# Kernel tuning notes

Measured on AMD Instinct MI355X. Metric: run time of the kernel, lower is better.

Reference implementation:

```python
import jax, jax.numpy as jnp
import numpy as np

ALPHA = 0.25
GAMMA = 2.0
DELTA = 0.5
BREAK_W = 1.0
REG_W = 1.0
CLASS_WEIGHT_TABLE = jnp.array([1.0, 4.0, 3.0, 2.0], dtype=jnp.float32)  # classes 0..3
LOG_CLAMP = -100.0  # torch BCELoss clamps log terms at -100

B, T = 2048, 16384


def setup_inputs() -> dict:
    key = jax.random.key(0)
    k1, k2, k3, k4 = jax.random.split(key, 4)
    break_predictions = jax.random.uniform(k1, (B, T), dtype=jnp.float32)
    regression_predictions = jax.random.uniform(k2, (B, T), dtype=jnp.float32) * 3.0
    break_targets = jax.random.uniform(k3, (B, T), dtype=jnp.float32)
    regression_targets = jax.random.uniform(k4, (B, T), dtype=jnp.float32) * 3.0
    return {
        "break_predictions": break_predictions,
        "regression_predictions": regression_predictions,
        "break_targets": break_targets,
        "regression_targets": regression_targets,
    }


def _bce(p, t):
    # torch BCELoss: mean of -(t*log(p) + (1-t)*log(1-p)), logs clamped at -100
    log_p = jnp.maximum(jnp.log(p), LOG_CLAMP)
    log_1p = jnp.maximum(jnp.log1p(-p), LOG_CLAMP)
    return jnp.mean(-(t * log_p + (1.0 - t) * log_1p))


def _duration_aware_focal(y_pred, y_true):
    y_pred = y_pred.reshape(-1)
    y_true = y_true.reshape(-1)
    # class-weight gather: round + clamp to [0,3], index a 4-entry table
    cls_idx = jnp.clip(jnp.round(y_true), 0.0, 3.0).astype(jnp.int32)
    weights = CLASS_WEIGHT_TABLE[cls_idx]
    d = jnp.abs(y_pred - y_true)
    focal = jnp.clip(d / DELTA, 0.0, 1.0) ** GAMMA
    # smooth L1 with beta=DELTA
    base = jnp.where(d < DELTA, 0.5 * d * d / DELTA, d - 0.5 * DELTA)
    return jnp.mean(ALPHA * focal * base * weights)


def reference(break_predictions, regression_predictions, break_targets, regression_targets):
    bt = jnp.clip(break_targets, 0.0, 1.0)
    bp = jnp.clip(break_predictions, 0.0, 1.0)
    break_loss = _bce(bp, bt)
    regression_loss = _duration_aware_focal(regression_predictions, regression_targets)
    total = BREAK_W * break_loss + REG_W * regression_loss
    return (total, break_loss, regression_loss)
```

## Files before the change

kernel.cpp:

```cpp
#include <hip/hip_runtime.h>


constexpr int BLOCK = 256;
constexpr int GRID  = 2048;

__device__ __forceinline__ void accum_elem(float pv, float tv, float qv, float sv,
                                           float& accB, float& accR) {
    constexpr float LN2 = 0.6931471805599453f;
    float pc = fminf(fmaxf(pv, 0.0f), 1.0f);
    float tc = fminf(fmaxf(tv, 0.0f), 1.0f);
    float lp  = fmaxf(__log2f(pc)        * LN2, -100.0f);
    float l1p = fmaxf(__log2f(1.0f - pc) * LN2, -100.0f);
    accB -= tc * lp + (1.0f - tc) * l1p;
    float d = fabsf(qv - sv);
    float f = fminf(d + d, 1.0f);
    float base = (d < 0.5f) ? (d * d) : (d - 0.25f);
    float r = fminf(fmaxf(__builtin_rintf(sv), 0.0f), 3.0f);
    float w = (r == 0.0f) ? 1.0f : (r == 1.0f) ? 4.0f : (r == 2.0f) ? 3.0f : 2.0f;
    accR += 0.25f * (f * f) * base * w;
}

__device__ __forceinline__ void accum4(const float4& p, const float4& t,
                                       const float4& q, const float4& s,
                                       float& accB0, float& accR0,
                                       float& accB1, float& accR1) {
    accum_elem(p.x, t.x, q.x, s.x, accB0, accR0);
    accum_elem(p.y, t.y, q.y, s.y, accB1, accR1);
    accum_elem(p.z, t.z, q.z, s.z, accB0, accR0);
    accum_elem(p.w, t.w, q.w, s.w, accB1, accR1);
}

__global__ __launch_bounds__(BLOCK) void partial_kernel(
    const float4* __restrict__ bp4, const float4* __restrict__ rp4,
    const float4* __restrict__ bt4, const float4* __restrict__ rt4,
    float* __restrict__ partials, int n4, int n)
{
    float accB0 = 0.0f, accR0 = 0.0f, accB1 = 0.0f, accR1 = 0.0f;
    const int stride = gridDim.x * blockDim.x;
    int i = blockIdx.x * blockDim.x + threadIdx.x;
    if (i < n4) {
        float4 p = bp4[i], q = rp4[i], t = bt4[i], s = rt4[i];
        int j = i + stride;
        #pragma unroll 2
        while (j < n4) {
            float4 pn = bp4[j], qn = rp4[j], tn = bt4[j], sn = rt4[j];
            accum4(p, t, q, s, accB0, accR0, accB1, accR1);
            p = pn; q = qn; t = tn; s = sn;
            j += stride;
        }
        accum4(p, t, q, s, accB0, accR0, accB1, accR1);
    }
    if (blockIdx.x == 0) {
        const float* bp = (const float*)bp4;
        const float* bt = (const float*)bt4;
        const float* rp = (const float*)rp4;
        const float* rt = (const float*)rt4;
        for (int k = n4 * 4 + threadIdx.x; k < n; k += BLOCK)
            accum_elem(bp[k], bt[k], rp[k], rt[k], accB0, accR0);
    }
    float accB = accB0 + accB1;
    float accR = accR0 + accR1;
    #pragma unroll
    for (int off = 32; off > 0; off >>= 1) {
        accB += __shfl_down(accB, off, 64);
        accR += __shfl_down(accR, off, 64);
    }
    __shared__ float sB[BLOCK / 64], sR[BLOCK / 64];
    const int lane = threadIdx.x & 63;
    const int wid  = threadIdx.x >> 6;
    if (lane == 0) { sB[wid] = accB; sR[wid] = accR; }
    __syncthreads();
    if (threadIdx.x == 0) {
        float b = 0.0f, r = 0.0f;
        #pragma unroll
        for (int w = 0; w < BLOCK / 64; ++w) { b += sB[w]; r += sR[w]; }
        partials[blockIdx.x]        = b;
        partials[GRID + blockIdx.x] = r;
    }
}

__global__ __launch_bounds__(BLOCK) void final_kernel(
    const float* __restrict__ partials, float* __restrict__ out, double invN)
{
    double accB = 0.0, accR = 0.0;
    for (int i = threadIdx.x; i < GRID; i += BLOCK) {
        accB += (double)partials[i];
        accR += (double)partials[GRID + i];
    }
    #pragma unroll
    for (int off = 32; off > 0; off >>= 1) {
        accB += __shfl_down(accB, off, 64);
        accR += __shfl_down(accR, off, 64);
    }
    __shared__ double dB[BLOCK / 64], dR[BLOCK / 64];
    const int lane = threadIdx.x & 63;
    const int wid  = threadIdx.x >> 6;
    if (lane == 0) { dB[wid] = accB; dR[wid] = accR; }
    __syncthreads();
    if (threadIdx.x == 0) {
        double b = 0.0, r = 0.0;
        #pragma unroll
        for (int w = 0; w < BLOCK / 64; ++w) { b += dB[w]; r += dR[w]; }
        const double bm = b * invN;
        const double rm = r * invN;
        out[0] = (float)(bm + rm);
        out[1] = (float)bm;
        out[2] = (float)rm;
    }
}

extern "C" void kernel_launch(void* const* d_in, const int* in_sizes, int n_in,
                              void* d_out, int out_size, void* d_ws, size_t ws_size,
                              hipStream_t stream) {
    const float* bp = (const float*)d_in[0];
    const float* rp = (const float*)d_in[1];
    const float* bt = (const float*)d_in[2];
    const float* rt = (const float*)d_in[3];
    const int n  = in_sizes[0];
    const int n4 = n / 4;
    float* partials = (float*)d_ws;

    partial_kernel<<<GRID, BLOCK, 0, stream>>>(
        (const float4*)bp, (const float4*)rp, (const float4*)bt, (const float4*)rt,
        partials, n4, n);
    final_kernel<<<1, BLOCK, 0, stream>>>(partials, (float*)d_out, 1.0 / (double)n);
}
```

Baseline: 104.6 us.

## Fuse final reduction into loss kernel via fixed-point atomics and last-block finish

Replaces the second reduction kernel with 64-bit fixed-point atomic accumulation and a last-block-done counter that writes the final outputs. A memset of the workspace is added before the launch. The per-element math moves the ln2 and 0.25 scale factors out of the inner loop and rewrites the BCE term with one fewer multiply. The streaming loop becomes a 2x explicit unroll instead of software-prefetch. The atomics add contention and quantization error, and the memset adds its own launch.

```diff
diff --git a/kernel.cpp b/kernel.cpp
--- a/kernel.cpp
+++ b/kernel.cpp
@@ -3,21 +3,23 @@
 
 constexpr int BLOCK = 256;
 constexpr int GRID  = 2048;
+constexpr double SCALE = 16777216.0;
+constexpr double LN2D  = 0.6931471805599453;
 
 __device__ __forceinline__ void accum_elem(float pv, float tv, float qv, float sv,
                                            float& accB, float& accR) {
-    constexpr float LN2 = 0.6931471805599453f;
+    constexpr float CLAMP2 = -144.26950408889634f;
     float pc = fminf(fmaxf(pv, 0.0f), 1.0f);
     float tc = fminf(fmaxf(tv, 0.0f), 1.0f);
-    float lp  = fmaxf(__log2f(pc)        * LN2, -100.0f);
-    float l1p = fmaxf(__log2f(1.0f - pc) * LN2, -100.0f);
-    accB -= tc * lp + (1.0f - tc) * l1p;
+    float lp  = fmaxf(__log2f(pc),        CLAMP2);
+    float l1p = fmaxf(__log2f(1.0f - pc), CLAMP2);
+    accB -= l1p + tc * (lp - l1p);
     float d = fabsf(qv - sv);
     float f = fminf(d + d, 1.0f);
     float base = (d < 0.5f) ? (d * d) : (d - 0.25f);
     float r = fminf(fmaxf(__builtin_rintf(sv), 0.0f), 3.0f);
     float w = (r == 0.0f) ? 1.0f : (r == 1.0f) ? 4.0f : (r == 2.0f) ? 3.0f : 2.0f;
-    accR += 0.25f * (f * f) * base * w;
+    accR += (f * f) * base * w;
 }
 
 __device__ __forceinline__ void accum4(const float4& p, const float4& t,
@@ -30,24 +32,23 @@
     accum_elem(p.w, t.w, q.w, s.w, accB1, accR1);
 }
 
-__global__ __launch_bounds__(BLOCK) void partial_kernel(
+__global__ __launch_bounds__(BLOCK) void loss_kernel(
     const float4* __restrict__ bp4, const float4* __restrict__ rp4,
     const float4* __restrict__ bt4, const float4* __restrict__ rt4,
-    float* __restrict__ partials, int n4, int n)
+    unsigned long long* __restrict__ ws,
+    float* __restrict__ out, int n4, int n, double invN)
 {
     float accB0 = 0.0f, accR0 = 0.0f, accB1 = 0.0f, accR1 = 0.0f;
-    const int stride = gridDim.x * blockDim.x;
-    int i = blockIdx.x * blockDim.x + threadIdx.x;
+    const int stride = GRID * BLOCK;
+    int i = blockIdx.x * BLOCK + threadIdx.x;
+    for (; i + stride < n4; i += 2 * stride) {
+        float4 p0 = bp4[i],          q0 = rp4[i],          t0 = bt4[i],          s0 = rt4[i];
+        float4 p1 = bp4[i + stride], q1 = rp4[i + stride], t1 = bt4[i + stride], s1 = rt4[i + stride];
+        accum4(p0, t0, q0, s0, accB0, accR0, accB1, accR1);
+        accum4(p1, t1, q1, s1, accB0, accR0, accB1, accR1);
+    }
     if (i < n4) {
         float4 p = bp4[i], q = rp4[i], t = bt4[i], s = rt4[i];
-        int j = i + stride;
-        #pragma unroll 2
-        while (j < n4) {
-            float4 pn = bp4[j], qn = rp4[j], tn = bt4[j], sn = rt4[j];
-            accum4(p, t, q, s, accB0, accR0, accB1, accR1);
-            p = pn; q = qn; t = tn; s = sn;
-            j += stride;
-        }
         accum4(p, t, q, s, accB0, accR0, accB1, accR1);
     }
     if (blockIdx.x == 0) {
@@ -74,38 +75,21 @@
         float b = 0.0f, r = 0.0f;
         #pragma unroll
         for (int w = 0; w < BLOCK / 64; ++w) { b += sB[w]; r += sR[w]; }
-        partials[blockIdx.x]        = b;
-        partials[GRID + blockIdx.x] = r;
-    }
-}
-
-__global__ __launch_bounds__(BLOCK) void final_kernel(
-    const float* __restrict__ partials, float* __restrict__ out, double invN)
-{
-    double accB = 0.0, accR = 0.0;
-    for (int i = threadIdx.x; i < GRID; i += BLOCK) {
-        accB += (double)partials[i];
-        accR += (double)partials[GRID + i];
-    }
-    #pragma unroll
-    for (int off = 32; off > 0; off >>= 1) {
-        accB += __shfl_down(accB, off, 64);
-        accR += __shfl_down(accR, off, 64);
-    }
-    __shared__ double dB[BLOCK / 64], dR[BLOCK / 64];
-    const int lane = threadIdx.x & 63;
-    const int wid  = threadIdx.x >> 6;
-    if (lane == 0) { dB[wid] = accB; dR[wid] = accR; }
-    __syncthreads();
-    if (threadIdx.x == 0) {
-        double b = 0.0, r = 0.0;
-        #pragma unroll
-        for (int w = 0; w < BLOCK / 64; ++w) { b += dB[w]; r += dR[w]; }
-        const double bm = b * invN;
-        const double rm = r * invN;
-        out[0] = (float)(bm + rm);
-        out[1] = (float)bm;
-        out[2] = (float)rm;
+        unsigned long long bq = (unsigned long long)(long long)llrint((double)b * LN2D  * SCALE);
+        unsigned long long rq = (unsigned long long)(long long)llrint((double)r * 0.25 * SCALE);
+        atomicAdd(&ws[0], bq);
+        atomicAdd(&ws[1], rq);
+        __threadfence();
+        unsigned long long prev = atomicAdd(&ws[2], 1ULL);
+        if (prev == (unsigned long long)(GRID - 1)) {
+            unsigned long long tb = atomicAdd(&ws[0], 0ULL);
+            unsigned long long tr = atomicAdd(&ws[1], 0ULL);
+            double bm = (double)(long long)tb / SCALE * invN;
+            double rm = (double)(long long)tr / SCALE * invN;
+            out[0] = (float)(bm + rm);
+            out[1] = (float)bm;
+            out[2] = (float)rm;
+        }
     }
 }
 
@@ -118,10 +102,10 @@
     const float* rt = (const float*)d_in[3];
     const int n  = in_sizes[0];
     const int n4 = n / 4;
-    float* partials = (float*)d_ws;
+    unsigned long long* ws = (unsigned long long*)d_ws;
 
-    partial_kernel<<<GRID, BLOCK, 0, stream>>>(
+    hipMemsetAsync(ws, 0, 3 * sizeof(unsigned long long), stream);
+    loss_kernel<<<GRID, BLOCK, 0, stream>>>(
         (const float4*)bp, (const float4*)rp, (const float4*)bt, (const float4*)rt,
-        partials, n4, n);
-    final_kernel<<<1, BLOCK, 0, stream>>>(partials, (float*)d_out, 1.0 / (double)n);
+        ws, (float*)d_out, n4, n, 1.0 / (double)n);
 }
```

Result: slower. 197.9 us (+89.2%).
